# Kernel tuning notes

Hardware: AMD Instinct MI355X
Metric: run time of the kernel (lower is better)

Reference implementation:

```python
import jax, jax.numpy as jnp
import numpy as np

B, L, S, H, E = 4, 2048, 2048, 8, 64

def setup_inputs() -> dict:
    key = jax.random.key(0)
    kq, kk, kv, kt, kd = jax.random.split(key, 5)
    return {
        "queries": jax.random.normal(kq, (B, L, H, E), dtype=jnp.float32),
        "keys": jax.random.normal(kk, (B, S, H, E), dtype=jnp.float32),
        "values": jax.random.normal(kv, (B, S, H, E), dtype=jnp.float32),
        "attn_mask": jnp.zeros((1,), dtype=bool),
        "tau": jax.random.uniform(kt, (B, 1), dtype=jnp.float32),
        "delta": jax.random.normal(kd, (B, 1), dtype=jnp.float32),
    }

def reference(queries, keys, values, attn_mask, tau, delta):
    # queries: [B,L,H,E], keys: [B,S,H,E], values: [B,S,H,D]
    Bq, Lq, Hq, Eq = queries.shape
    scale = 1.0 / jnp.sqrt(jnp.float32(Eq))
    scores = jnp.einsum('blhe,bshe->bhls', queries, keys)  # [B,H,L,S]
    scores = scores * tau.reshape(Bq, 1, 1, 1)             # per-batch tau scale
    scores = scores + delta.reshape(Bq, 1, 1, 1)           # per-batch delta bias
    A = jax.nn.softmax(scale * scores, axis=-1)            # dropout is identity at eval
    V = jnp.einsum('bhls,bshd->blhd', A, values)           # [B,L,H,D]
    return V
```

## Files before the change

### kernel.cpp

```cpp
#include <hip/hip_runtime.h>
#include <hip/hip_bf16.h>
#include <stdint.h>

#define LL 2048
#define SS 2048
#define HH 8
#define EE 64
#define RSG 512

typedef float v4f  __attribute__((ext_vector_type(4)));
typedef float v16f __attribute__((ext_vector_type(16)));
typedef short s4v  __attribute__((ext_vector_type(4)));
typedef short s8v  __attribute__((ext_vector_type(8)));

__device__ __forceinline__ short f2bf(float f) {
    unsigned u = __float_as_uint(f);
    u = (u + 0x7fffu + ((u >> 16) & 1u)) >> 16;
    return (short)u;
}

__device__ __forceinline__ s4v pack4bf(float a, float b, float c, float d) {
    float2 ab = make_float2(a, b), cd = make_float2(c, d);
    __hip_bfloat162 r0 = __float22bfloat162_rn(ab);
    __hip_bfloat162 r1 = __float22bfloat162_rn(cd);
    s4v r;
    __builtin_memcpy(&r, &r0, 4);
    __builtin_memcpy(((char*)&r) + 4, &r1, 4);
    return r;
}

__global__ __launch_bounds__(256)
void dsattn_prep(const float* __restrict__ kk, const float* __restrict__ vv,
                 short* __restrict__ kimg, short* __restrict__ vimg)
{
    __shared__ float T[64][68];
    const int t = threadIdx.x;
    const int blk = blockIdx.x;
    if (blk < 1024) {
        const int vb = blk;
        const int b = vb >> 8, h = (vb >> 5) & 7, ts = vb & 31;
        const float* kp = kk + ((size_t)b * SS + ts * 64) * RSG + h * EE;
        #pragma unroll
        for (int c = 0; c < 4; ++c) {
            int idx = c * 256 + t, s = idx >> 4, e0 = (idx & 15) << 2;
            *(v4f*)&T[s][e0] = *(const v4f*)(kp + (size_t)s * RSG + e0);
        }
        __syncthreads();
        short* dst = kimg + (size_t)vb * 4096;
        #pragma unroll
        for (int half = 0; half < 2; ++half) {
            int ci = half * 256 + t;
            int echunk = ci >> 6, srow = ci & 63;
            s8v ov;
            #pragma unroll
            for (int j = 0; j < 8; ++j) ov[j] = f2bf(T[srow][echunk * 8 + j]);
            *(s8v*)(dst + ci * 8) = ov;
        }
    } else {
        const int vb = blk - 1024;
        const int b = vb >> 8, h = (vb >> 5) & 7, ts = vb & 31;
        const float* vp = vv + ((size_t)b * SS + ts * 64) * RSG + h * EE;
        #pragma unroll
        for (int c = 0; c < 4; ++c) {
            int idx = c * 256 + t, s = idx >> 4, e0 = (idx & 15) << 2;
            *(v4f*)&T[s][e0] = *(const v4f*)(vp + (size_t)s * RSG + e0);
        }
        __syncthreads();
        short* dst = vimg + (size_t)vb * 4096;
        #pragma unroll
        for (int half = 0; half < 2; ++half) {
            int ci = half * 256 + t;
            int c = ci >> 6, e = ci & 63;
            int sbase = 16 * (c >> 1) + 4 * (c & 1);
            s8v ov;
            #pragma unroll
            for (int j = 0; j < 8; ++j) {
                int s = sbase + 8 * (j >> 2) + (j & 3);
                ov[j] = f2bf(T[s][e]);
            }
            *(s8v*)(dst + ci * 8) = ov;
        }
    }
}

__global__ __launch_bounds__(512, 4)
void dsattn_main(const float* __restrict__ q, const short* __restrict__ kimg,
                 const short* __restrict__ vimg, const float* __restrict__ tau,
                 float* __restrict__ out)
{
    __shared__ short KV[2][2][8192];

    const int t    = threadIdx.x;
    const int lane = t & 63;
    const int w    = t >> 6;
    const int w4   = w & 3;
    const int grp  = w >> 2;
    const int l31  = lane & 31;
    const int hi   = lane >> 5;

    const int hw = blockIdx.x;
    const int wu = (hw & 7) * 64 + (hw >> 3);
    const int mt = wu & 15;
    const int h  = (wu >> 4) & 7;
    const int b  = wu >> 7;

    const float scf = 0.125f * 1.44269504088896f * tau[b];

    s8v qf[4];
    {
        const float* qb = q + ((size_t)b * LL + (size_t)mt * 128 + w4 * 32 + l31) * RSG
                            + h * EE + 8 * hi;
        #pragma unroll
        for (int ks = 0; ks < 4; ++ks) {
            v4f a0 = *(const v4f*)(qb + 16 * ks);
            v4f a1 = *(const v4f*)(qb + 16 * ks + 4);
            s4v p0 = pack4bf(a0[0] * scf, a0[1] * scf, a0[2] * scf, a0[3] * scf);
            s4v p1 = pack4bf(a1[0] * scf, a1[1] * scf, a1[2] * scf, a1[3] * scf);
            s8v f;
            #pragma unroll
            for (int j = 0; j < 4; ++j) { f[j] = p0[j]; f[4 + j] = p1[j]; }
            qf[ks] = f;
        }
    }

    const char* gsrc;
    {
        const size_t pan  = (size_t)((b * 8 + h) * 32) * 8192;
        const size_t soff = (size_t)grp * 16 * 8192;
        if (w4 < 2) gsrc = (const char*)kimg + pan + soff + w4 * 4096 + lane * 16;
        else        gsrc = (const char*)vimg + pan + soff + (w4 - 2) * 4096 + lane * 16;
    }

    #define STAGE(slot)                                                                   \
        {                                                                                 \
            _Pragma("unroll")                                                             \
            for (int j = 0; j < 4; ++j) {                                                 \
                __builtin_amdgcn_global_load_lds(                                         \
                    (const __attribute__((address_space(1))) unsigned*)(gsrc + j * 1024), \
                    (__attribute__((address_space(3))) unsigned*)&KV[grp][slot][w4 * 2048 + j * 512], \
                    16, 0, 0);                                                            \
            }                                                                             \
            gsrc += 8192;                                                                 \
        }

    v16f oacc[2];
    #pragma unroll
    for (int mb = 0; mb < 2; ++mb)
        #pragma unroll
        for (int r = 0; r < 16; ++r) oacc[mb][r] = 0.0f;
    float rsum = 0.0f;

    const int rb = hi * 512 + l31 * 8;

    asm volatile("s_waitcnt vmcnt(0)" ::: "memory");
    __builtin_amdgcn_sched_barrier(0);
    STAGE(0);
    STAGE(1);

    #pragma unroll 1
    for (int sw = 0; sw < 16; ++sw) {
        const int p = sw & 1;

        __builtin_amdgcn_sched_barrier(0);
        if (sw <= 14) asm volatile("s_waitcnt vmcnt(4)" ::: "memory");
        else          asm volatile("s_waitcnt vmcnt(0)" ::: "memory");
        __builtin_amdgcn_s_barrier();
        __builtin_amdgcn_sched_barrier(0);

        const short* Kp = &KV[grp][p][0];
        const short* Vp = &KV[grp][p][4096];

        v16f st[2];
        #pragma unroll
        for (int mb = 0; mb < 2; ++mb) {
            v16f z;
            #pragma unroll
            for (int r = 0; r < 16; ++r) z[r] = 0.0f;
            #pragma unroll
            for (int ks = 0; ks < 4; ++ks) {
                s8v kf = *(const s8v*)&Kp[ks * 1024 + mb * 256 + rb];
                z = __builtin_amdgcn_mfma_f32_32x32x16_bf16(kf, qf[ks], z, 0, 0, 0);
            }
            st[mb] = z;
        }

        #pragma unroll
        for (int mb = 0; mb < 2; ++mb)
            #pragma unroll
            for (int r = 0; r < 16; ++r)
                st[mb][r] = __builtin_amdgcn_exp2f(st[mb][r]);
        float s0 = 0.f, s1 = 0.f;
        #pragma unroll
        for (int r = 0; r < 16; ++r) { s0 += st[0][r]; s1 += st[1][r]; }
        rsum += s0 + s1;

        s8v pf[4];
        #pragma unroll
        for (int tt = 0; tt < 4; ++tt) {
            int o = 8 * (tt & 1);
            const v16f& sv = st[tt >> 1];
            s4v lo = pack4bf(sv[o + 0], sv[o + 1], sv[o + 2], sv[o + 3]);
            s4v hs = pack4bf(sv[o + 4], sv[o + 5], sv[o + 6], sv[o + 7]);
            s8v f;
            #pragma unroll
            for (int j = 0; j < 4; ++j) { f[j] = lo[j]; f[4 + j] = hs[j]; }
            pf[tt] = f;
        }

        #pragma unroll
        for (int mb = 0; mb < 2; ++mb) {
            v16f acc = oacc[mb];
            #pragma unroll
            for (int ks = 0; ks < 4; ++ks) {
                s8v vf = *(const s8v*)&Vp[ks * 1024 + mb * 256 + rb];
                acc = __builtin_amdgcn_mfma_f32_32x32x16_bf16(vf, pf[ks], acc, 0, 0, 0);
            }
            oacc[mb] = acc;
        }

        if (sw <= 13) {
            __builtin_amdgcn_sched_barrier(0);
            __builtin_amdgcn_s_barrier();
            __builtin_amdgcn_sched_barrier(0);
            STAGE(p);
        }
    }

    __syncthreads();
    float* sh = (float*)&KV[0][0][0];
    const int slot = (t & 255) * 33;
    if (grp == 1) {
        #pragma unroll
        for (int mb = 0; mb < 2; ++mb)
            #pragma unroll
            for (int r = 0; r < 16; ++r) sh[slot + mb * 16 + r] = oacc[mb][r];
        sh[slot + 32] = rsum;
    }
    __syncthreads();
    if (grp == 0) {
        #pragma unroll
        for (int mb = 0; mb < 2; ++mb)
            #pragma unroll
            for (int r = 0; r < 16; ++r) oacc[mb][r] += sh[slot + mb * 16 + r];
        rsum += sh[slot + 32];
        rsum += __shfl_xor(rsum, 32);
        const float inv = 1.0f / rsum;
        float* ob = out + ((size_t)b * LL + (size_t)mt * 128 + w4 * 32 + l31) * RSG + h * EE;
        #pragma unroll
        for (int mb = 0; mb < 2; ++mb)
            #pragma unroll
            for (int rq = 0; rq < 4; ++rq) {
                int e0 = 32 * mb + 8 * rq + 4 * hi;
                v4f o4 = { oacc[mb][4 * rq + 0] * inv, oacc[mb][4 * rq + 1] * inv,
                           oacc[mb][4 * rq + 2] * inv, oacc[mb][4 * rq + 3] * inv };
                *(v4f*)(ob + e0) = o4;
            }
    }
}

extern "C" void kernel_launch(void* const* d_in, const int* in_sizes, int n_in,
                              void* d_out, int out_size, void* d_ws, size_t ws_size,
                              hipStream_t stream) {
    const float* q     = (const float*)d_in[0];
    const float* k     = (const float*)d_in[1];
    const float* v     = (const float*)d_in[2];
    const float* tau   = (const float*)d_in[4];
    float* out = (float*)d_out;

    short* kimg = (short*)d_ws;
    short* vimg = kimg + (size_t)4 * SS * RSG;

    dsattn_prep<<<dim3(2048), dim3(256), 0, stream>>>(k, v, kimg, vimg);
    dsattn_main<<<dim3(512), dim3(512), 0, stream>>>(q, kimg, vimg, tau, out);
}
```

Measured before the change: 135.3 us.

## Load K fragments directly from global bf16 and stage only V in LDS

The prep kernel now converts K to bf16 in its original row-major layout instead of building a tiled image, and the main kernel reads K MFMA operands straight from global memory. Only V goes through the async LDS double buffer, which halves the shared-memory footprint and the waitcnt depth. The epilogue reduction is split into two passes to fit the smaller LDS buffer. The aim is to raise occupancy and cut LDS traffic, at the cost of strided, uncached-in-LDS global K loads that sit on the critical path before the QK MFMAs.

```diff
diff --git a/kernel.cpp b/kernel.cpp
--- a/kernel.cpp
+++ b/kernel.cpp
@@ -31,30 +31,18 @@
 
 __global__ __launch_bounds__(256)
 void dsattn_prep(const float* __restrict__ kk, const float* __restrict__ vv,
-                 short* __restrict__ kimg, short* __restrict__ vimg)
+                 short* __restrict__ kbf, short* __restrict__ vimg)
 {
     __shared__ float T[64][68];
     const int t = threadIdx.x;
     const int blk = blockIdx.x;
     if (blk < 1024) {
-        const int vb = blk;
-        const int b = vb >> 8, h = (vb >> 5) & 7, ts = vb & 31;
-        const float* kp = kk + ((size_t)b * SS + ts * 64) * RSG + h * EE;
+        const float* src = kk + (size_t)blk * 4096;
+        short* dst = kbf + (size_t)blk * 4096;
         #pragma unroll
         for (int c = 0; c < 4; ++c) {
-            int idx = c * 256 + t, s = idx >> 4, e0 = (idx & 15) << 2;
-            *(v4f*)&T[s][e0] = *(const v4f*)(kp + (size_t)s * RSG + e0);
-        }
-        __syncthreads();
-        short* dst = kimg + (size_t)vb * 4096;
-        #pragma unroll
-        for (int half = 0; half < 2; ++half) {
-            int ci = half * 256 + t;
-            int echunk = ci >> 6, srow = ci & 63;
-            s8v ov;
-            #pragma unroll
-            for (int j = 0; j < 8; ++j) ov[j] = f2bf(T[srow][echunk * 8 + j]);
-            *(s8v*)(dst + ci * 8) = ov;
+            v4f d = *(const v4f*)(src + (c * 256 + t) * 4);
+            *(s4v*)(dst + (c * 256 + t) * 4) = pack4bf(d[0], d[1], d[2], d[3]);
         }
     } else {
         const int vb = blk - 1024;
@@ -84,11 +72,11 @@
 }
 
 __global__ __launch_bounds__(512, 4)
-void dsattn_main(const float* __restrict__ q, const short* __restrict__ kimg,
+void dsattn_main(const float* __restrict__ q, const short* __restrict__ kbf,
                  const short* __restrict__ vimg, const float* __restrict__ tau,
                  float* __restrict__ out)
 {
-    __shared__ short KV[2][2][8192];
+    __shared__ short KV[2][2][4096];
 
     const int t    = threadIdx.x;
     const int lane = t & 63;
@@ -123,21 +111,20 @@
         }
     }
 
-    const char* gsrc;
-    {
-        const size_t pan  = (size_t)((b * 8 + h) * 32) * 8192;
-        const size_t soff = (size_t)grp * 16 * 8192;
-        if (w4 < 2) gsrc = (const char*)kimg + pan + soff + w4 * 4096 + lane * 16;
-        else        gsrc = (const char*)vimg + pan + soff + (w4 - 2) * 4096 + lane * 16;
-    }
+    const short* kg = kbf + ((size_t)b * SS + grp * 1024 + (size_t)l31) * RSG
+                          + h * EE + hi * 8;
+
+    const char* gsrc = (const char*)vimg
+                     + ((size_t)((b * 8 + h) * 32 + grp * 16)) * 8192
+                     + w4 * 1024 + lane * 16;
 
     #define STAGE(slot)                                                                   \
         {                                                                                 \
             _Pragma("unroll")                                                             \
-            for (int j = 0; j < 4; ++j) {                                                 \
+            for (int j = 0; j < 2; ++j) {                                                 \
                 __builtin_amdgcn_global_load_lds(                                         \
-                    (const __attribute__((address_space(1))) unsigned*)(gsrc + j * 1024), \
-                    (__attribute__((address_space(3))) unsigned*)&KV[grp][slot][w4 * 2048 + j * 512], \
+                    (const __attribute__((address_space(1))) unsigned*)(gsrc + j * 4096), \
+                    (__attribute__((address_space(3))) unsigned*)&KV[grp][slot][w4 * 512 + j * 2048], \
                     16, 0, 0);                                                            \
             }                                                                             \
             gsrc += 8192;                                                                 \
@@ -162,13 +149,12 @@
         const int p = sw & 1;
 
         __builtin_amdgcn_sched_barrier(0);
-        if (sw <= 14) asm volatile("s_waitcnt vmcnt(4)" ::: "memory");
+        if (sw <= 14) asm volatile("s_waitcnt vmcnt(2)" ::: "memory");
         else          asm volatile("s_waitcnt vmcnt(0)" ::: "memory");
         __builtin_amdgcn_s_barrier();
         __builtin_amdgcn_sched_barrier(0);
 
-        const short* Kp = &KV[grp][p][0];
-        const short* Vp = &KV[grp][p][4096];
+        const short* Vp = &KV[grp][p][0];
 
         v16f st[2];
         #pragma unroll
@@ -178,21 +164,25 @@
             for (int r = 0; r < 16; ++r) z[r] = 0.0f;
             #pragma unroll
             for (int ks = 0; ks < 4; ++ks) {
-                s8v kf = *(const s8v*)&Kp[ks * 1024 + mb * 256 + rb];
+                s8v kf = *(const s8v*)(kg + (size_t)(mb * 32) * RSG + ks * 16);
                 z = __builtin_amdgcn_mfma_f32_32x32x16_bf16(kf, qf[ks], z, 0, 0, 0);
             }
             st[mb] = z;
         }
+        kg += (size_t)64 * RSG;
 
         #pragma unroll
         for (int mb = 0; mb < 2; ++mb)
             #pragma unroll
             for (int r = 0; r < 16; ++r)
                 st[mb][r] = __builtin_amdgcn_exp2f(st[mb][r]);
-        float s0 = 0.f, s1 = 0.f;
-        #pragma unroll
-        for (int r = 0; r < 16; ++r) { s0 += st[0][r]; s1 += st[1][r]; }
-        rsum += s0 + s1;
+        float sx = 0.f, sy = 0.f;
+        #pragma unroll
+        for (int r = 0; r < 16; r += 2) {
+            sx += st[0][r]     + st[1][r];
+            sy += st[0][r + 1] + st[1][r + 1];
+        }
+        rsum += sx + sy;
 
         s8v pf[4];
         #pragma unroll
@@ -228,21 +218,29 @@
 
     __syncthreads();
     float* sh = (float*)&KV[0][0][0];
-    const int slot = (t & 255) * 33;
+    const int tid = t & 255;
+    const int slot = tid * 17;
     if (grp == 1) {
         #pragma unroll
-        for (int mb = 0; mb < 2; ++mb)
-            #pragma unroll
-            for (int r = 0; r < 16; ++r) sh[slot + mb * 16 + r] = oacc[mb][r];
-        sh[slot + 32] = rsum;
+        for (int r = 0; r < 16; ++r) sh[slot + r] = oacc[0][r];
+        sh[slot + 16] = rsum;
     }
     __syncthreads();
     if (grp == 0) {
         #pragma unroll
-        for (int mb = 0; mb < 2; ++mb)
-            #pragma unroll
-            for (int r = 0; r < 16; ++r) oacc[mb][r] += sh[slot + mb * 16 + r];
-        rsum += sh[slot + 32];
+        for (int r = 0; r < 16; ++r) oacc[0][r] += sh[slot + r];
+        rsum += sh[slot + 16];
+    }
+    __syncthreads();
+    if (grp == 1) {
+        #pragma unroll
+        for (int r = 0; r < 16; ++r) sh[slot + r] = oacc[1][r];
+    }
+    __syncthreads();
+    if (grp == 0) {
+        #pragma unroll
+        for (int r = 0; r < 16; ++r) oacc[1][r] += sh[slot + r];
+
         rsum += __shfl_xor(rsum, 32);
         const float inv = 1.0f / rsum;
         float* ob = out + ((size_t)b * LL + (size_t)mt * 128 + w4 * 32 + l31) * RSG + h * EE;
@@ -267,9 +265,9 @@
     const float* tau   = (const float*)d_in[4];
     float* out = (float*)d_out;
 
-    short* kimg = (short*)d_ws;
-    short* vimg = kimg + (size_t)4 * SS * RSG;
-
-    dsattn_prep<<<dim3(2048), dim3(256), 0, stream>>>(k, v, kimg, vimg);
-    dsattn_main<<<dim3(512), dim3(512), 0, stream>>>(q, kimg, vimg, tau, out);
-}
+    short* kbf  = (short*)d_ws;
+    short* vimg = kbf + (size_t)4 * SS * RSG;
+
+    dsattn_prep<<<dim3(2048), dim3(256), 0, stream>>>(k, v, kbf, vimg);
+    dsattn_main<<<dim3(512), dim3(512), 0, stream>>>(q, kbf, vimg, tau, out);
+}
```

Result: slower. 170.7 us (+26.2%).

## Split S-range across separate blocks with atomic-counter cross-block reduction

Applied to the files above, without the earlier changes.

The main kernel previously split the key range between two 4-wave groups inside one 512-thread block and reduced through LDS. Now each half of the key range runs in its own 256-thread block, giving 1024 smaller blocks. The two blocks of a pair combine through global memory: whichever finishes first writes its partial output and row sums, and the second spin-waits on a counter, adds them and normalises. This aims for finer scheduling granularity and less LDS per block. In exchange it adds global round-trips, a spin-wait that assumes both blocks of a pair run concurrently, and counter resets done in the prep kernel.

```diff
diff --git a/kernel.cpp b/kernel.cpp
--- a/kernel.cpp
+++ b/kernel.cpp
@@ -31,11 +31,13 @@
 
 __global__ __launch_bounds__(256)
 void dsattn_prep(const float* __restrict__ kk, const float* __restrict__ vv,
-                 short* __restrict__ kimg, short* __restrict__ vimg)
+                 short* __restrict__ kimg, short* __restrict__ vimg,
+                 unsigned* __restrict__ ctrb)
 {
     __shared__ float T[64][68];
     const int t = threadIdx.x;
     const int blk = blockIdx.x;
+    if (blk < 4) { ctrb[blk * 256 + t] = 0u; }
     if (blk < 1024) {
         const int vb = blk;
         const int b = vb >> 8, h = (vb >> 5) & 7, ts = vb & 31;
@@ -83,32 +85,33 @@
     }
 }
 
-__global__ __launch_bounds__(512, 4)
+__global__ __launch_bounds__(256, 4)
 void dsattn_main(const float* __restrict__ q, const short* __restrict__ kimg,
                  const short* __restrict__ vimg, const float* __restrict__ tau,
-                 float* __restrict__ out)
+                 float* __restrict__ out, float* __restrict__ rsumb,
+                 unsigned* __restrict__ ctrb)
 {
-    __shared__ short KV[2][2][8192];
+    __shared__ short KV[2][8192];
+    __shared__ int role;
 
     const int t    = threadIdx.x;
     const int lane = t & 63;
     const int w    = t >> 6;
-    const int w4   = w & 3;
-    const int grp  = w >> 2;
     const int l31  = lane & 31;
     const int hi   = lane >> 5;
 
     const int hw = blockIdx.x;
-    const int wu = (hw & 7) * 64 + (hw >> 3);
-    const int mt = wu & 15;
-    const int h  = (wu >> 4) & 7;
-    const int b  = wu >> 7;
+    const int wu = (hw & 7) * 128 + (hw >> 3);
+    const int sh = wu & 1;
+    const int mt = (wu >> 1) & 15;
+    const int h  = (wu >> 5) & 7;
+    const int b  = wu >> 8;
 
     const float scf = 0.125f * 1.44269504088896f * tau[b];
 
     s8v qf[4];
     {
-        const float* qb = q + ((size_t)b * LL + (size_t)mt * 128 + w4 * 32 + l31) * RSG
+        const float* qb = q + ((size_t)b * LL + (size_t)mt * 128 + w * 32 + l31) * RSG
                             + h * EE + 8 * hi;
         #pragma unroll
         for (int ks = 0; ks < 4; ++ks) {
@@ -125,10 +128,9 @@
 
     const char* gsrc;
     {
-        const size_t pan  = (size_t)((b * 8 + h) * 32) * 8192;
-        const size_t soff = (size_t)grp * 16 * 8192;
-        if (w4 < 2) gsrc = (const char*)kimg + pan + soff + w4 * 4096 + lane * 16;
-        else        gsrc = (const char*)vimg + pan + soff + (w4 - 2) * 4096 + lane * 16;
+        const size_t base = ((size_t)((b * 8 + h) * 32 + sh * 16)) * 8192;
+        if (w < 2) gsrc = (const char*)kimg + base + w * 4096 + lane * 16;
+        else       gsrc = (const char*)vimg + base + (w - 2) * 4096 + lane * 16;
     }
 
     #define STAGE(slot)                                                                   \
@@ -137,7 +139,7 @@
             for (int j = 0; j < 4; ++j) {                                                 \
                 __builtin_amdgcn_global_load_lds(                                         \
                     (const __attribute__((address_space(1))) unsigned*)(gsrc + j * 1024), \
-                    (__attribute__((address_space(3))) unsigned*)&KV[grp][slot][w4 * 2048 + j * 512], \
+                    (__attribute__((address_space(3))) unsigned*)&KV[slot][w * 2048 + j * 512], \
                     16, 0, 0);                                                            \
             }                                                                             \
             gsrc += 8192;                                                                 \
@@ -167,8 +169,8 @@
         __builtin_amdgcn_s_barrier();
         __builtin_amdgcn_sched_barrier(0);
 
-        const short* Kp = &KV[grp][p][0];
-        const short* Vp = &KV[grp][p][4096];
+        const short* Kp = &KV[p][0];
+        const short* Vp = &KV[p][4096];
 
         v16f st[2];
         #pragma unroll
@@ -226,26 +228,49 @@
         }
     }
 
+    const int pair = wu >> 1;
+    unsigned* ctr = ctrb + pair * 2;
+    float* rws = rsumb + (size_t)pair * 256;
+    float* ob = out + ((size_t)b * LL + (size_t)mt * 128 + w * 32 + l31) * RSG + h * EE;
+
     __syncthreads();
-    float* sh = (float*)&KV[0][0][0];
-    const int slot = (t & 255) * 33;
-    if (grp == 1) {
+    if (t == 0) role = (int)atomicAdd(&ctr[0], 1u);
+    __syncthreads();
+
+    if (role == 0) {
         #pragma unroll
         for (int mb = 0; mb < 2; ++mb)
             #pragma unroll
-            for (int r = 0; r < 16; ++r) sh[slot + mb * 16 + r] = oacc[mb][r];
-        sh[slot + 32] = rsum;
-    }
-    __syncthreads();
-    if (grp == 0) {
+            for (int rq = 0; rq < 4; ++rq) {
+                int e0 = 32 * mb + 8 * rq + 4 * hi;
+                v4f o4 = { oacc[mb][4 * rq + 0], oacc[mb][4 * rq + 1],
+                           oacc[mb][4 * rq + 2], oacc[mb][4 * rq + 3] };
+                *(v4f*)(ob + e0) = o4;
+            }
+        rws[t] = rsum;
+        __syncthreads();
+        __threadfence();
+        if (t == 0) atomicAdd(&ctr[1], 1u);
+    } else {
+        if (t == 0) {
+            while (atomicAdd(&ctr[1], 0u) == 0u) __builtin_amdgcn_s_sleep(2);
+        }
+        __syncthreads();
+        __threadfence();
+        rsum += rws[t];
         #pragma unroll
         for (int mb = 0; mb < 2; ++mb)
             #pragma unroll
-            for (int r = 0; r < 16; ++r) oacc[mb][r] += sh[slot + mb * 16 + r];
-        rsum += sh[slot + 32];
+            for (int rq = 0; rq < 4; ++rq) {
+                int e0 = 32 * mb + 8 * rq + 4 * hi;
+                v4f pp = *(const v4f*)(ob + e0);
+                oacc[mb][4 * rq + 0] += pp[0];
+                oacc[mb][4 * rq + 1] += pp[1];
+                oacc[mb][4 * rq + 2] += pp[2];
+                oacc[mb][4 * rq + 3] += pp[3];
+            }
         rsum += __shfl_xor(rsum, 32);
         const float inv = 1.0f / rsum;
-        float* ob = out + ((size_t)b * LL + (size_t)mt * 128 + w4 * 32 + l31) * RSG + h * EE;
         #pragma unroll
         for (int mb = 0; mb < 2; ++mb)
             #pragma unroll
@@ -267,9 +292,11 @@
     const float* tau   = (const float*)d_in[4];
     float* out = (float*)d_out;
 
-    short* kimg = (short*)d_ws;
-    short* vimg = kimg + (size_t)4 * SS * RSG;
-
-    dsattn_prep<<<dim3(2048), dim3(256), 0, stream>>>(k, v, kimg, vimg);
-    dsattn_main<<<dim3(512), dim3(512), 0, stream>>>(q, kimg, vimg, tau, out);
-}
+    short*    kimg  = (short*)d_ws;
+    short*    vimg  = kimg + (size_t)4 * SS * RSG;
+    float*    rsumb = (float*)(vimg + (size_t)4 * SS * RSG);
+    unsigned* ctrb  = (unsigned*)(rsumb + (size_t)512 * 256);
+
+    dsattn_prep<<<dim3(2048), dim3(256), 0, stream>>>(k, v, kimg, vimg, ctrb);
+    dsattn_main<<<dim3(1024), dim3(256), 0, stream>>>(q, kimg, vimg, tau, out, rsumb, ctrb);
+}
```

Result: slower. 278.6 us (+105.9%).
